# Kernel optimization log

Hardware: AMD Instinct MI355X
Metric: run time of the kernel (lower is better)

The kernel has to match this reference:

```python
import jax, jax.numpy as jnp
import jax.lax as lax
import numpy as np

# ---- Parallel3DGeometry constants ----
B, C = 1, 1
D, H, W = 64, 96, 96          # internal volume layout (z, y, x)
V, U, A = 64, 96, 90          # detector rows, detector cols, projection angles
SX = SY = SD = 1.0            # voxel size (x, y, z)
SU = SV = 1.0                 # detector spacing
NSTEPS = H + W + 2            # upper bound on voxels crossed by an XY ray
DIAG = float(np.sqrt(SX * SX + SY * SY))
EPS = 1e-12


def _t_for(p0, dp, pmin, pmax):
    # slab entry/exit parameters, matching torch _t_for (incl. parallel-ray cases)
    par = jnp.abs(dp) < EPS
    safe = jnp.where(par, 1.0, dp)
    t0 = (pmin - p0) / safe
    t1 = (pmax - p0) / safe
    lo = jnp.minimum(t0, t1)
    hi = jnp.maximum(t0, t1)
    inside = (p0 >= pmin) & (p0 <= pmax)
    lo = jnp.where(par, jnp.where(inside, -jnp.inf, jnp.inf), lo)
    hi = jnp.where(par, jnp.where(inside, jnp.inf, -jnp.inf), hi)
    return lo, hi


def _trace():
    """Vectorized Siddon XY traversal for all A*U rays.

    Returns Is, Js (int32 [A,U,NSTEPS]) voxel indices and Ws (f32 [A,U,NSTEPS])
    segment lengths (0 where the ray has exited / padded steps).
    """
    angles = jnp.linspace(0.0, np.pi, A, endpoint=False).astype(jnp.float32)
    cos_t = jnp.cos(angles)
    sin_t = jnp.sin(angles)
    u = (jnp.arange(U, dtype=jnp.float32) - (U - 1) / 2.0) * SU
    dx = jnp.broadcast_to(cos_t[:, None], (A, U)).reshape(-1)
    dy = jnp.broadcast_to(sin_t[:, None], (A, U)).reshape(-1)
    x0 = (-u[None, :] * sin_t[:, None]).reshape(-1)
    y0 = (u[None, :] * cos_t[:, None]).reshape(-1)

    x_min = -((W - 1) / 2.0) * SX; x_max = ((W - 1) / 2.0) * SX
    y_min = -((H - 1) / 2.0) * SY; y_max = ((H - 1) / 2.0) * SY
    tx0, tx1 = _t_for(x0, dx, x_min, x_max)
    ty0, ty1 = _t_for(y0, dy, y_min, y_max)
    t_entry = jnp.maximum(tx0, ty0)
    t_exit = jnp.minimum(tx1, ty1)
    alive0 = t_entry < t_exit
    te = jnp.where(alive0, t_entry, 0.0)
    tex = jnp.where(alive0, t_exit, 0.0)
    xe = x0 + te * dx
    ye = y0 + te * dy
    i0 = jnp.clip(jnp.round(xe / SX + (W - 1) / 2.0), 0, W - 1).astype(jnp.int32)
    j0 = jnp.clip(jnp.round(ye / SY + (H - 1) / 2.0), 0, H - 1).astype(jnp.int32)
    cxw = (W - 1) / 2.0 * SX
    cyh = (H - 1) / 2.0 * SY

    def body(st, _):
        i, j, x, y, t, alive = st
        valid = alive & (t < tex - EPS)
        fi = i.astype(jnp.float32)
        fj = j.astype(jnp.float32)
        xn = jnp.where(dx > 0, (fi + 0.5) * SX - cxw,
                       jnp.where(dx < 0, (fi - 0.5) * SX - cxw, jnp.inf))
        yn = jnp.where(dy > 0, (fj + 0.5) * SY - cyh,
                       jnp.where(dy < 0, (fj - 0.5) * SY - cyh, jnp.inf))
        okx = jnp.abs(dx) > EPS
        oky = jnp.abs(dy) > EPS
        tx = jnp.where(okx, (xn - x) / jnp.where(okx, dx, 1.0), jnp.inf)
        ty = jnp.where(oky, (yn - y) / jnp.where(oky, dy, 1.0), jnp.inf)
        dt = jnp.minimum(jnp.minimum(tx, ty), tex - t)
        seg = jnp.maximum(0.0, dt * DIAG / jnp.maximum(jnp.abs(dx) + jnp.abs(dy), EPS))
        w = jnp.where(valid, seg, 0.0)
        i_n = i + jnp.where(tx <= ty, jnp.where(dx > 0, 1, -1), 0)
        j_n = j + jnp.where(ty <= tx, jnp.where(dy > 0, 1, -1), 0)
        inb = (i_n >= 0) & (i_n < W) & (j_n >= 0) & (j_n < H)
        dts = jnp.where(valid, dt, 0.0)
        st2 = (jnp.where(valid, i_n, i), jnp.where(valid, j_n, j),
               x + dx * dts, y + dy * dts, t + dts, valid & inb)
        return st2, (i, j, w)

    init = (i0, j0, xe, ye, te, alive0)
    _, (Is, Js, Ws) = lax.scan(body, init, None, length=NSTEPS)
    # [NSTEPS, R] -> [A, U, NSTEPS]
    Is = Is.T.reshape(A, U, NSTEPS)
    Js = Js.T.reshape(A, U, NSTEPS)
    Ws = Ws.T.reshape(A, U, NSTEPS)
    return Is, Js, Ws


def _forward(vol):
    # model-facing [B,C,X,Y,Z] -> internal [B,C,D,H,W]
    vol_int = jnp.transpose(vol, (0, 1, 4, 3, 2))
    Is, Js, Ws = _trace()
    v_phys = (jnp.arange(V, dtype=jnp.float32) - (V - 1) / 2.0) * SV
    k = jnp.clip(jnp.round(v_phys / SD + (D - 1) / 2.0), 0, D - 1).astype(jnp.int32)
    # gather voxel values along every ray: [B,C,V,A,U,NSTEPS]
    g = vol_int[:, :, k[:, None, None, None], Js[None], Is[None]]
    out = jnp.einsum('bcvaun,aun->bcvau', g, Ws.astype(vol.dtype))
    # internal [B,C,V,A,U] (== out[b,c,a,v,u] reordered) -> model-facing [B,C,U,A,V]
    return jnp.transpose(out, (0, 1, 4, 3, 2))


def setup_inputs() -> dict:
    key = jax.random.key(0)
    vol = jax.random.normal(key, (B, C, W, H, D), dtype=jnp.float32)
    return {"vol": vol}


def reference(vol):
    return _forward(vol)
```

## Files before the change

kernel.cpp:

```cpp
#include <hip/hip_runtime.h>
#include <math.h>

namespace {
constexpr int NA = 90, NU = 96, NV = 64, NW = 96, NH = 96, ND = 64;
constexpr int NRAY   = NA * NU;
constexpr int NENT   = 256;
constexpr int CNTMAX = 208;
constexpr int TILE   = 8;
constexpr int NBLK   = 1024;
constexpr int NEXTRA = NRAY - NBLK * TILE;
}

__device__ inline void sincos_poly(double xd, float* s, float* c)
{
    const double INV_PIO2 = 0.63661977236758134308;
    const double PIO2_HI  = 1.57079632679489655800e+00;
    const double PIO2_LO  = 6.12323399573676603587e-17;
    const double qd = rint(xd * INV_PIO2);
    const double r  = (xd - qd * PIO2_HI) - qd * PIO2_LO;
    const double z  = r * r;
    const double sp = r + (r * z) * (-1.66666666666666324348e-01 + z *
                     ( 8.33333333332248946124e-03 + z *
                     (-1.98412698298579493134e-04 + z *
                     ( 2.75573137070700676789e-06 + z *
                     (-2.50507602534068634195e-08 + z *
                       1.58969099521155010221e-10)))));
    const double cp = 1.0 + z * (-0.5 + z *
                     ( 4.16666666666666019037e-02 + z *
                     (-1.38888888888741095749e-03 + z *
                     ( 2.48015872894767294178e-05 + z *
                     (-2.75573143513906633035e-07 + z *
                     ( 2.08757232129817482790e-09 + z *
                      -1.13596475577881948265e-11))))));
    const int q = (int)qd;
    const double sv = (q == 0) ? sp : ((q == 1) ? cp : -sp);
    const double cv = (q == 0) ? cp : ((q == 1) ? -sp : -cp);
    *s = (float)sv;
    *c = (float)cv;
}

__device__ __forceinline__ float rflf(float x) {
    return __int_as_float(__builtin_amdgcn_readfirstlane(__float_as_int(x)));
}
__device__ __forceinline__ int rfli(int x) {
    return __builtin_amdgcn_readfirstlane(x);
}

__device__ __forceinline__ void do_ray(const float* __restrict__ vol,
                                       float* __restrict__ out,
                                       int2* __restrict__ myRow,
                                       const int ray, const int lane)
{
    const int a = ray / NU;
    const int u = ray - a * NU;

    const float EPSf = 1e-12f;
    const float INFp = __builtin_inff();
    const float DIAG = 1.41421356237309514547f;

    const float ang = (float)a * (float)(3.14159265358979323846 / 90.0);
    float dy, dx;
    sincos_poly((double)ang, &dy, &dx);
    const float uu = (float)u - 47.5f;
    const float x0 = __fmul_rn(-uu, dy);
    const float y0 = __fmul_rn( uu, dx);

    const float xmin = -47.5f, xmax = 47.5f;
    const float ymin = -47.5f, ymax = 47.5f;

    float tx0, tx1;
    {
        const bool par = fabsf(dx) < EPSf;
        const float safe = par ? 1.0f : dx;
        const float t0 = __fdiv_rn(xmin - x0, safe);
        const float t1 = __fdiv_rn(xmax - x0, safe);
        const float lo = fminf(t0, t1), hi = fmaxf(t0, t1);
        const bool inside = (x0 >= xmin) && (x0 <= xmax);
        tx0 = par ? (inside ? -INFp : INFp) : lo;
        tx1 = par ? (inside ?  INFp : -INFp) : hi;
    }
    float ty0, ty1;
    {
        const bool par = fabsf(dy) < EPSf;
        const float safe = par ? 1.0f : dy;
        const float t0 = __fdiv_rn(ymin - y0, safe);
        const float t1 = __fdiv_rn(ymax - y0, safe);
        const float lo = fminf(t0, t1), hi = fmaxf(t0, t1);
        const bool inside = (y0 >= ymin) && (y0 <= ymax);
        ty0 = par ? (inside ? -INFp : INFp) : lo;
        ty1 = par ? (inside ?  INFp : -INFp) : hi;
    }

    const float t_entry = fmaxf(tx0, ty0);
    const float t_exit  = fminf(tx1, ty1);
    const bool  alive0  = t_entry < t_exit;
    const float te  = rflf(alive0 ? t_entry : 0.0f);
    const float tex = rflf(alive0 ? t_exit  : 0.0f);

    const float xe = __fadd_rn(x0, __fmul_rn(te, dx));
    const float ye = __fadd_rn(y0, __fmul_rn(te, dy));
    const int i0 = rfli((int)fminf(fmaxf(rintf(__fadd_rn(xe, 47.5f)), 0.0f), 95.0f));
    const int j0 = rfli((int)fminf(fmaxf(rintf(__fadd_rn(ye, 47.5f)), 0.0f), 95.0f));

    const bool okx = fabsf(dx) > EPSf;
    const bool oky = fabsf(dy) > EPSf;
    const float inv_dx = okx ? __fdiv_rn(1.0f, dx) : 0.0f;
    const float inv_dy = oky ? __fdiv_rn(1.0f, dy) : 0.0f;
    const float wscale = rflf(__fdiv_rn(DIAG, fmaxf(fabsf(dx) + fabsf(dy), EPSf)));
    const float tex_m_eps = rflf(__fadd_rn(tex, -EPSf));

    const float cx = (dx > 0.0f) ? -47.0f : -48.0f;
    const float cy = (dy > 0.0f) ? -47.0f : -48.0f;
    const float Ax = rflf(okx ? __fadd_rn(te, __fmul_rn(((float)i0 + cx) - xe, inv_dx)) : INFp);
    const float Ay = rflf(oky ? __fadd_rn(te, __fmul_rn(((float)j0 + cy) - ye, inv_dy)) : INFp);
    const float px = rflf(okx ? fabsf(inv_dx) : 0.0f);
    const float py = rflf(oky ? fabsf(inv_dy) : 0.0f);
    const int   si = rfli((dx > 0.0f) ? 1 : -1);
    const int   sj = rfli((dy > 0.0f) ? 1 : -1);

    const float inv_pq = rflf(__fdiv_rn(1.0f, px + py));
    const float Cc = rflf(Ay - Ax);

    int nx = 0, ny = 0;
    if (okx) {
        const float Qx = __fdiv_rn(tex_m_eps - Ax, px);
        nx = min(96, max(0, (int)floorf(Qx) + 1));
    }
    if (oky) {
        const float Qy = __fdiv_rn(tex_m_eps - Ay, py);
        ny = min(96, max(0, (int)floorf(Qy) + 1));
    }
    const int nvalid = 1 + nx + ny;
    const int rounds = rfli(alive0 ? min(4, (nvalid + 2 + 63) >> 6) : 0);

    int cnt = 0;
    for (int rnd = 0; rnd < rounds; ++rnd) {
        const int n = (rnd << 6) + lane;
        const float nf = (float)n;

        float kf = __fmul_rn(__fmaf_rn(nf, py, Cc), inv_pq);
        kf = fminf(fmaxf(kf, 0.0f), nf);
        int k = (int)rintf(kf);

        #pragma unroll
        for (int it = 0; it < 4; ++it) {
            const int m = n - k;
            const float Txk   = __fmaf_rn((float)k, px, Ax);
            const float Txkm1 = (k > 0) ? __fmaf_rn((float)(k - 1), px, Ax) : -INFp;
            const float Tyl   = __fmaf_rn((float)m, py, Ay);
            const float Tylm1 = (m > 0) ? __fmaf_rn((float)(m - 1), py, Ay) : -INFp;
            const bool dec = (Txkm1 > Tyl);
            const bool inc = (!dec) && (Tylm1 > Txk);
            k += inc ? 1 : (dec ? -1 : 0);
        }

        const int m = n - k;
        const float Txk   = __fmaf_rn((float)k, px, Ax);
        const float Txkm1 = (k > 0) ? __fmaf_rn((float)(k - 1), px, Ax) : -INFp;
        const float Tyl   = __fmaf_rn((float)m, py, Ay);
        const float Tylm1 = (m > 0) ? __fmaf_rn((float)(m - 1), py, Ay) : -INFp;

        const float Tn   = fminf(Txk, Tyl);
        const float prev = fmaxf(te, fmaxf(Txkm1, Tylm1));
        const float dt   = __fadd_rn(fminf(Tn, tex), -fminf(prev, tex));
        const bool active = (prev < tex_m_eps);
        float w = __fmul_rn(fmaxf(0.0f, dt), wscale);
        w = active ? w : 0.0f;

        const int ii = min(95, max(0, i0 + ((si > 0) ? k : -k)));
        const int jj = min(95, max(0, j0 + ((sj > 0) ? m : -m)));
        int2 e;
        e.x = (ii * NH + jj) << 8;
        e.y = __float_as_int(w);
        myRow[n] = e;

        cnt += (int)__popcll(__ballot(active));
    }
    const int cap = min((cnt + 15) & ~15, CNTMAX);

    const int r   = lane >> 4;
    const int sub = lane & 15;
    const int subOff = sub << 4;

    const int2* __restrict__ eRow = myRow + r;
    const char* __restrict__ vb   = (const char*)vol;

    float4 acc[4] = {{0,0,0,0}, {0,0,0,0}, {0,0,0,0}, {0,0,0,0}};
    if (cap > 0) {
        int2 e0 = eRow[0];
        int2 e1 = eRow[4];
        int2 e2 = eRow[8];
        int2 e3 = eRow[12];
        float4 v0 = *(const float4*)(vb + (e0.x + subOff));
        float4 v1 = *(const float4*)(vb + (e1.x + subOff));
        float4 v2 = *(const float4*)(vb + (e2.x + subOff));
        float4 v3 = *(const float4*)(vb + (e3.x + subOff));

        for (int n = 16; n < cap; n += 16) {
            const int2 f0 = eRow[n];
            const int2 f1 = eRow[n + 4];
            const int2 f2 = eRow[n + 8];
            const int2 f3 = eRow[n + 12];
            const float4 u0 = *(const float4*)(vb + (f0.x + subOff));
            const float4 u1 = *(const float4*)(vb + (f1.x + subOff));
            const float4 u2 = *(const float4*)(vb + (f2.x + subOff));
            const float4 u3 = *(const float4*)(vb + (f3.x + subOff));

            const float w0 = __int_as_float(e0.y);
            const float w1 = __int_as_float(e1.y);
            const float w2 = __int_as_float(e2.y);
            const float w3 = __int_as_float(e3.y);
            acc[0].x = fmaf(w0, v0.x, acc[0].x); acc[0].y = fmaf(w0, v0.y, acc[0].y);
            acc[0].z = fmaf(w0, v0.z, acc[0].z); acc[0].w = fmaf(w0, v0.w, acc[0].w);
            acc[1].x = fmaf(w1, v1.x, acc[1].x); acc[1].y = fmaf(w1, v1.y, acc[1].y);
            acc[1].z = fmaf(w1, v1.z, acc[1].z); acc[1].w = fmaf(w1, v1.w, acc[1].w);
            acc[2].x = fmaf(w2, v2.x, acc[2].x); acc[2].y = fmaf(w2, v2.y, acc[2].y);
            acc[2].z = fmaf(w2, v2.z, acc[2].z); acc[2].w = fmaf(w2, v2.w, acc[2].w);
            acc[3].x = fmaf(w3, v3.x, acc[3].x); acc[3].y = fmaf(w3, v3.y, acc[3].y);
            acc[3].z = fmaf(w3, v3.z, acc[3].z); acc[3].w = fmaf(w3, v3.w, acc[3].w);

            e0 = f0; e1 = f1; e2 = f2; e3 = f3;
            v0 = u0; v1 = u1; v2 = u2; v3 = u3;
        }

        const float w0 = __int_as_float(e0.y);
        const float w1 = __int_as_float(e1.y);
        const float w2 = __int_as_float(e2.y);
        const float w3 = __int_as_float(e3.y);
        acc[0].x = fmaf(w0, v0.x, acc[0].x); acc[0].y = fmaf(w0, v0.y, acc[0].y);
        acc[0].z = fmaf(w0, v0.z, acc[0].z); acc[0].w = fmaf(w0, v0.w, acc[0].w);
        acc[1].x = fmaf(w1, v1.x, acc[1].x); acc[1].y = fmaf(w1, v1.y, acc[1].y);
        acc[1].z = fmaf(w1, v1.z, acc[1].z); acc[1].w = fmaf(w1, v1.w, acc[1].w);
        acc[2].x = fmaf(w2, v2.x, acc[2].x); acc[2].y = fmaf(w2, v2.y, acc[2].y);
        acc[2].z = fmaf(w2, v2.z, acc[2].z); acc[2].w = fmaf(w2, v2.w, acc[2].w);
        acc[3].x = fmaf(w3, v3.x, acc[3].x); acc[3].y = fmaf(w3, v3.y, acc[3].y);
        acc[3].z = fmaf(w3, v3.z, acc[3].z); acc[3].w = fmaf(w3, v3.w, acc[3].w);
    }

    float sx = (acc[0].x + acc[1].x) + (acc[2].x + acc[3].x);
    float sy = (acc[0].y + acc[1].y) + (acc[2].y + acc[3].y);
    float sz = (acc[0].z + acc[1].z) + (acc[2].z + acc[3].z);
    float sw = (acc[0].w + acc[1].w) + (acc[2].w + acc[3].w);

    sx += __shfl_xor(sx, 16, 64);  sy += __shfl_xor(sy, 16, 64);
    sz += __shfl_xor(sz, 16, 64);  sw += __shfl_xor(sw, 16, 64);
    sx += __shfl_xor(sx, 32, 64);  sy += __shfl_xor(sy, 32, 64);
    sz += __shfl_xor(sz, 32, 64);  sw += __shfl_xor(sw, 32, 64);

    if (lane < 16) {
        float4 res; res.x = sx; res.y = sy; res.z = sz; res.w = sw;
        *(float4*)(out + (u * NA + a) * NV + (sub << 2)) = res;
    }
}

__global__ __launch_bounds__(512, 8)
void siddon_fused(const float* __restrict__ vol, float* __restrict__ out)
{
    __shared__ int2 sEnt[TILE][NENT];

    const int tid  = threadIdx.x;
    const int wid  = tid >> 6;
    const int lane = tid & 63;
    const int bid  = blockIdx.x;

    int2* __restrict__ myRow = &sEnt[wid][0];

    const int ray0 = bid * TILE + wid;
    do_ray(vol, out, myRow, ray0, lane);

    if (bid < NEXTRA && wid == ((bid + (bid >> 8)) & 7)) {
        do_ray(vol, out, myRow, NBLK * TILE + bid, lane);
    }
}

extern "C" void kernel_launch(void* const* d_in, const int* in_sizes, int n_in,
                              void* d_out, int out_size, void* d_ws, size_t ws_size,
                              hipStream_t stream) {
    const float* vol = (const float*)d_in[0];
    float* out = (float*)d_out;
    hipLaunchKernelGGL(siddon_fused, dim3(NBLK), dim3(512), 0, stream, vol, out);
}
```

Measured before the change: 67.29 us.

## Split leftover-ray gather across all warps with shared-memory reduction

Blocks that own one of the leftover rays no longer give that whole ray to a single warp. Every warp now traces the extra ray into a shared row, and each warp gathers a strided subset of its 16-entry chunks. Partial sums are reduced through shared memory after a block barrier. The aim is to shorten the tail where one warp per block did twice the work. The cost is redundant tracing of the extra ray by all eight warps, plus a barrier and extra shared memory.

```diff
diff --git a/kernel.cpp b/kernel.cpp
--- a/kernel.cpp
+++ b/kernel.cpp
@@ -46,10 +46,8 @@
     return __builtin_amdgcn_readfirstlane(x);
 }
 
-__device__ __forceinline__ void do_ray(const float* __restrict__ vol,
-                                       float* __restrict__ out,
-                                       int2* __restrict__ myRow,
-                                       const int ray, const int lane)
+__device__ __forceinline__ int trace_ray(int2* __restrict__ myRow,
+                                         const int ray, const int lane)
 {
     const int a = ray / NU;
     const int u = ray - a * NU;
@@ -176,100 +174,147 @@
 
         cnt += (int)__popcll(__ballot(active));
     }
-    const int cap = min((cnt + 15) & ~15, CNTMAX);
-
-    const int r   = lane >> 4;
-    const int sub = lane & 15;
-    const int subOff = sub << 4;
-
-    const int2* __restrict__ eRow = myRow + r;
-    const char* __restrict__ vb   = (const char*)vol;
-
-    float4 acc[4] = {{0,0,0,0}, {0,0,0,0}, {0,0,0,0}, {0,0,0,0}};
-    if (cap > 0) {
-        int2 e0 = eRow[0];
-        int2 e1 = eRow[4];
-        int2 e2 = eRow[8];
-        int2 e3 = eRow[12];
-        float4 v0 = *(const float4*)(vb + (e0.x + subOff));
-        float4 v1 = *(const float4*)(vb + (e1.x + subOff));
-        float4 v2 = *(const float4*)(vb + (e2.x + subOff));
-        float4 v3 = *(const float4*)(vb + (e3.x + subOff));
-
-        for (int n = 16; n < cap; n += 16) {
-            const int2 f0 = eRow[n];
-            const int2 f1 = eRow[n + 4];
-            const int2 f2 = eRow[n + 8];
-            const int2 f3 = eRow[n + 12];
-            const float4 u0 = *(const float4*)(vb + (f0.x + subOff));
-            const float4 u1 = *(const float4*)(vb + (f1.x + subOff));
-            const float4 u2 = *(const float4*)(vb + (f2.x + subOff));
-            const float4 u3 = *(const float4*)(vb + (f3.x + subOff));
-
-            const float w0 = __int_as_float(e0.y);
-            const float w1 = __int_as_float(e1.y);
-            const float w2 = __int_as_float(e2.y);
-            const float w3 = __int_as_float(e3.y);
-            acc[0].x = fmaf(w0, v0.x, acc[0].x); acc[0].y = fmaf(w0, v0.y, acc[0].y);
-            acc[0].z = fmaf(w0, v0.z, acc[0].z); acc[0].w = fmaf(w0, v0.w, acc[0].w);
-            acc[1].x = fmaf(w1, v1.x, acc[1].x); acc[1].y = fmaf(w1, v1.y, acc[1].y);
-            acc[1].z = fmaf(w1, v1.z, acc[1].z); acc[1].w = fmaf(w1, v1.w, acc[1].w);
-            acc[2].x = fmaf(w2, v2.x, acc[2].x); acc[2].y = fmaf(w2, v2.y, acc[2].y);
-            acc[2].z = fmaf(w2, v2.z, acc[2].z); acc[2].w = fmaf(w2, v2.w, acc[2].w);
-            acc[3].x = fmaf(w3, v3.x, acc[3].x); acc[3].y = fmaf(w3, v3.y, acc[3].y);
-            acc[3].z = fmaf(w3, v3.z, acc[3].z); acc[3].w = fmaf(w3, v3.w, acc[3].w);
-
-            e0 = f0; e1 = f1; e2 = f2; e3 = f3;
-            v0 = u0; v1 = u1; v2 = u2; v3 = u3;
-        }
-
-        const float w0 = __int_as_float(e0.y);
-        const float w1 = __int_as_float(e1.y);
-        const float w2 = __int_as_float(e2.y);
-        const float w3 = __int_as_float(e3.y);
-        acc[0].x = fmaf(w0, v0.x, acc[0].x); acc[0].y = fmaf(w0, v0.y, acc[0].y);
-        acc[0].z = fmaf(w0, v0.z, acc[0].z); acc[0].w = fmaf(w0, v0.w, acc[0].w);
-        acc[1].x = fmaf(w1, v1.x, acc[1].x); acc[1].y = fmaf(w1, v1.y, acc[1].y);
-        acc[1].z = fmaf(w1, v1.z, acc[1].z); acc[1].w = fmaf(w1, v1.w, acc[1].w);
-        acc[2].x = fmaf(w2, v2.x, acc[2].x); acc[2].y = fmaf(w2, v2.y, acc[2].y);
-        acc[2].z = fmaf(w2, v2.z, acc[2].z); acc[2].w = fmaf(w2, v2.w, acc[2].w);
-        acc[3].x = fmaf(w3, v3.x, acc[3].x); acc[3].y = fmaf(w3, v3.y, acc[3].y);
-        acc[3].z = fmaf(w3, v3.z, acc[3].z); acc[3].w = fmaf(w3, v3.w, acc[3].w);
-    }
-
-    float sx = (acc[0].x + acc[1].x) + (acc[2].x + acc[3].x);
-    float sy = (acc[0].y + acc[1].y) + (acc[2].y + acc[3].y);
-    float sz = (acc[0].z + acc[1].z) + (acc[2].z + acc[3].z);
-    float sw = (acc[0].w + acc[1].w) + (acc[2].w + acc[3].w);
-
-    sx += __shfl_xor(sx, 16, 64);  sy += __shfl_xor(sy, 16, 64);
-    sz += __shfl_xor(sz, 16, 64);  sw += __shfl_xor(sw, 16, 64);
-    sx += __shfl_xor(sx, 32, 64);  sy += __shfl_xor(sy, 32, 64);
-    sz += __shfl_xor(sz, 32, 64);  sw += __shfl_xor(sw, 32, 64);
-
-    if (lane < 16) {
-        float4 res; res.x = sx; res.y = sy; res.z = sz; res.w = sw;
-        *(float4*)(out + (u * NA + a) * NV + (sub << 2)) = res;
-    }
-}
+    return min((cnt + 15) & ~15, CNTMAX);
+}
+
+#define CHUNK_FMA(E0,E1,E2,E3,V0,V1,V2,V3)                                        \
+    {                                                                             \
+        const float w0 = __int_as_float((E0).y);                                  \
+        const float w1 = __int_as_float((E1).y);                                  \
+        const float w2 = __int_as_float((E2).y);                                  \
+        const float w3 = __int_as_float((E3).y);                                  \
+        acc[0].x = fmaf(w0, (V0).x, acc[0].x); acc[0].y = fmaf(w0, (V0).y, acc[0].y); \
+        acc[0].z = fmaf(w0, (V0).z, acc[0].z); acc[0].w = fmaf(w0, (V0).w, acc[0].w); \
+        acc[1].x = fmaf(w1, (V1).x, acc[1].x); acc[1].y = fmaf(w1, (V1).y, acc[1].y); \
+        acc[1].z = fmaf(w1, (V1).z, acc[1].z); acc[1].w = fmaf(w1, (V1).w, acc[1].w); \
+        acc[2].x = fmaf(w2, (V2).x, acc[2].x); acc[2].y = fmaf(w2, (V2).y, acc[2].y); \
+        acc[2].z = fmaf(w2, (V2).z, acc[2].z); acc[2].w = fmaf(w2, (V2).w, acc[2].w); \
+        acc[3].x = fmaf(w3, (V3).x, acc[3].x); acc[3].y = fmaf(w3, (V3).y, acc[3].y); \
+        acc[3].z = fmaf(w3, (V3).z, acc[3].z); acc[3].w = fmaf(w3, (V3).w, acc[3].w); \
+    }
 
 __global__ __launch_bounds__(512, 8)
 void siddon_fused(const float* __restrict__ vol, float* __restrict__ out)
 {
-    __shared__ int2 sEnt[TILE][NENT];
+    __shared__ int2 sEnt[TILE + 1][NENT];
+    __shared__ float sPart[TILE][16][4];
 
     const int tid  = threadIdx.x;
     const int wid  = tid >> 6;
     const int lane = tid & 63;
     const int bid  = blockIdx.x;
 
-    int2* __restrict__ myRow = &sEnt[wid][0];
-
-    const int ray0 = bid * TILE + wid;
-    do_ray(vol, out, myRow, ray0, lane);
-
-    if (bid < NEXTRA && wid == ((bid + (bid >> 8)) & 7)) {
-        do_ray(vol, out, myRow, NBLK * TILE + bid, lane);
+    const int r   = lane >> 4;
+    const int sub = lane & 15;
+    const int subOff = sub << 4;
+    const char* __restrict__ vb = (const char*)vol;
+
+    {
+        int2* __restrict__ myRow = &sEnt[wid][0];
+        const int ray = bid * TILE + wid;
+        const int cap = trace_ray(myRow, ray, lane);
+        const int a = ray / NU;
+        const int u = ray - a * NU;
+
+        const int2* __restrict__ eRow = myRow + r;
+
+        float4 acc[4] = {{0,0,0,0}, {0,0,0,0}, {0,0,0,0}, {0,0,0,0}};
+        if (cap > 0) {
+            int2 e0 = eRow[0];
+            int2 e1 = eRow[4];
+            int2 e2 = eRow[8];
+            int2 e3 = eRow[12];
+            float4 v0 = *(const float4*)(vb + (e0.x + subOff));
+            float4 v1 = *(const float4*)(vb + (e1.x + subOff));
+            float4 v2 = *(const float4*)(vb + (e2.x + subOff));
+            float4 v3 = *(const float4*)(vb + (e3.x + subOff));
+
+            for (int n = 16; n < cap; n += 16) {
+                const int2 f0 = eRow[n];
+                const int2 f1 = eRow[n + 4];
+                const int2 f2 = eRow[n + 8];
+                const int2 f3 = eRow[n + 12];
+                const float4 u0 = *(const float4*)(vb + (f0.x + subOff));
+                const float4 u1 = *(const float4*)(vb + (f1.x + subOff));
+                const float4 u2 = *(const float4*)(vb + (f2.x + subOff));
+                const float4 u3 = *(const float4*)(vb + (f3.x + subOff));
+
+                CHUNK_FMA(e0, e1, e2, e3, v0, v1, v2, v3);
+
+                e0 = f0; e1 = f1; e2 = f2; e3 = f3;
+                v0 = u0; v1 = u1; v2 = u2; v3 = u3;
+            }
+            CHUNK_FMA(e0, e1, e2, e3, v0, v1, v2, v3);
+        }
+
+        float sx = (acc[0].x + acc[1].x) + (acc[2].x + acc[3].x);
+        float sy = (acc[0].y + acc[1].y) + (acc[2].y + acc[3].y);
+        float sz = (acc[0].z + acc[1].z) + (acc[2].z + acc[3].z);
+        float sw = (acc[0].w + acc[1].w) + (acc[2].w + acc[3].w);
+
+        sx += __shfl_xor(sx, 16, 64);  sy += __shfl_xor(sy, 16, 64);
+        sz += __shfl_xor(sz, 16, 64);  sw += __shfl_xor(sw, 16, 64);
+        sx += __shfl_xor(sx, 32, 64);  sy += __shfl_xor(sy, 32, 64);
+        sz += __shfl_xor(sz, 32, 64);  sw += __shfl_xor(sw, 32, 64);
+
+        if (lane < 16) {
+            float4 res; res.x = sx; res.y = sy; res.z = sz; res.w = sw;
+            *(float4*)(out + (u * NA + a) * NV + (sub << 2)) = res;
+        }
+    }
+
+    if (bid < NEXTRA) {
+        const int exray = NBLK * TILE + bid;
+        int2* __restrict__ xRowBase = &sEnt[TILE][0];
+        const int cap2 = trace_ray(xRowBase, exray, lane);
+
+        const int2* __restrict__ xRow = xRowBase + r;
+
+        float4 acc[4] = {{0,0,0,0}, {0,0,0,0}, {0,0,0,0}, {0,0,0,0}};
+        for (int n = (wid << 4); n < cap2; n += 128) {
+            const int2 e0 = xRow[n];
+            const int2 e1 = xRow[n + 4];
+            const int2 e2 = xRow[n + 8];
+            const int2 e3 = xRow[n + 12];
+            const float4 v0 = *(const float4*)(vb + (e0.x + subOff));
+            const float4 v1 = *(const float4*)(vb + (e1.x + subOff));
+            const float4 v2 = *(const float4*)(vb + (e2.x + subOff));
+            const float4 v3 = *(const float4*)(vb + (e3.x + subOff));
+            CHUNK_FMA(e0, e1, e2, e3, v0, v1, v2, v3);
+        }
+
+        float sx = (acc[0].x + acc[1].x) + (acc[2].x + acc[3].x);
+        float sy = (acc[0].y + acc[1].y) + (acc[2].y + acc[3].y);
+        float sz = (acc[0].z + acc[1].z) + (acc[2].z + acc[3].z);
+        float sw = (acc[0].w + acc[1].w) + (acc[2].w + acc[3].w);
+
+        sx += __shfl_xor(sx, 16, 64);  sy += __shfl_xor(sy, 16, 64);
+        sz += __shfl_xor(sz, 16, 64);  sw += __shfl_xor(sw, 16, 64);
+        sx += __shfl_xor(sx, 32, 64);  sy += __shfl_xor(sy, 32, 64);
+        sz += __shfl_xor(sz, 32, 64);  sw += __shfl_xor(sw, 32, 64);
+
+        if (lane < 16) {
+            sPart[wid][sub][0] = sx;
+            sPart[wid][sub][1] = sy;
+            sPart[wid][sub][2] = sz;
+            sPart[wid][sub][3] = sw;
+        }
+        __syncthreads();
+
+        if (wid == 0 && lane < 16) {
+            float rx = 0.0f, ry = 0.0f, rz = 0.0f, rw = 0.0f;
+            #pragma unroll
+            for (int w = 0; w < TILE; ++w) {
+                rx += sPart[w][sub][0];
+                ry += sPart[w][sub][1];
+                rz += sPart[w][sub][2];
+                rw += sPart[w][sub][3];
+            }
+            const int a2 = exray / NU;
+            const int u2 = exray - a2 * NU;
+            float4 res; res.x = rx; res.y = ry; res.z = rz; res.w = rw;
+            *(float4*)(out + (u2 * NA + a2) * NV + (sub << 2)) = res;
+        }
     }
 }
 
```

Result: slower. 69.42 us (+3.2%).
